# Kernel tuning notes

Hardware: AMD Instinct MI355X
Metric: run time of the kernel (lower is better)

Reference implementation:

```python
import jax, jax.numpy as jnp
from jax import lax
import numpy as np

SEQ, BATCH, IN, H = 512, 256, 180, 8


def _lstm_layer(x, w_ih, w_hh, b_ih, b_hh):
    # x: [S, B, I]; PyTorch gate order: i, f, g, o stacked along 4H
    S, B, _ = x.shape
    Hh = w_hh.shape[1]
    # input contribution for all timesteps at once (one big GEMM)
    xg = jnp.einsum('sbi,gi->sbg', x, w_ih) + b_ih + b_hh  # [S, B, 4H]

    def step(carry, xt):
        h, c = carry
        g = xt + h @ w_hh.T  # [B, 4H]
        i, f, gg, o = jnp.split(g, 4, axis=-1)
        i = jax.nn.sigmoid(i)
        f = jax.nn.sigmoid(f)
        gg = jnp.tanh(gg)
        o = jax.nn.sigmoid(o)
        c = f * c + i * gg
        h = o * jnp.tanh(c)
        return (h, c), h

    init = (jnp.zeros((B, Hh), x.dtype), jnp.zeros((B, Hh), x.dtype))
    _, ys = lax.scan(step, init, xg)
    return ys  # [S, B, H]


def setup_inputs() -> dict:
    key = jax.random.key(0)
    ks = jax.random.split(key, 11)
    s = 1.0 / np.sqrt(H)  # PyTorch LSTM init scale
    return {
        'x': jax.random.normal(ks[0], (SEQ, BATCH, IN), jnp.float32),
        'w_ih0': jax.random.uniform(ks[1], (4 * H, IN), jnp.float32, -s, s),
        'w_hh0': jax.random.uniform(ks[2], (4 * H, H), jnp.float32, -s, s),
        'b_ih0': jax.random.uniform(ks[3], (4 * H,), jnp.float32, -s, s),
        'b_hh0': jax.random.uniform(ks[4], (4 * H,), jnp.float32, -s, s),
        'w_ih1': jax.random.uniform(ks[5], (4 * H, H), jnp.float32, -s, s),
        'w_hh1': jax.random.uniform(ks[6], (4 * H, H), jnp.float32, -s, s),
        'b_ih1': jax.random.uniform(ks[7], (4 * H,), jnp.float32, -s, s),
        'b_hh1': jax.random.uniform(ks[8], (4 * H,), jnp.float32, -s, s),
        'w_reg': jax.random.uniform(ks[9], (2, H), jnp.float32, -s, s),
        'b_reg': jax.random.uniform(ks[10], (2,), jnp.float32, -s, s),
    }


def reference(x, w_ih0, w_hh0, b_ih0, b_hh0, w_ih1, w_hh1, b_ih1, b_hh1, w_reg, b_reg):
    h1 = _lstm_layer(x, w_ih0, w_hh0, b_ih0, b_hh0)   # [S, B, H]
    h2 = _lstm_layer(h1, w_ih1, w_hh1, b_ih1, b_hh1)  # [S, B, H]
    S, B, Hh = h2.shape
    flat = h2.reshape(S * B, Hh)
    return flat @ w_reg.T + b_reg  # [S*B, 2]
```

## Files before the change

kernel.cpp:

```cpp
#include <hip/hip_runtime.h>

#define S_  512
#define B_  256
#define NIN 180

typedef float v2 __attribute__((ext_vector_type(2)));

#define SSIG  -1.4426950408889634f
#define STANH -2.8853900817779268f

#define QP_X1 0xB1
#define QP_X2 0x4E
#define QP_X3 0x1B
#define ROR4  0x124
#define ROR8  0x128

template<int CTRL>
__device__ __forceinline__ float dppf(float x) {
    return __uint_as_float((unsigned)__builtin_amdgcn_update_dpp(
        0, (int)__float_as_uint(x), CTRL, 0xF, 0xF, true));
}

#define ROTS8(h, r) do { \
    r[0] = (h); \
    r[1] = dppf<QP_X1>(h); \
    r[2] = dppf<QP_X2>(h); \
    r[3] = dppf<QP_X3>(h); \
    r[4] = dppf<ROR4>(h); \
    r[5] = dppf<QP_X1>(r[4]); \
    r[6] = dppf<QP_X2>(r[4]); \
    r[7] = dppf<QP_X3>(r[4]); \
} while (0)

__global__ __launch_bounds__(512) void xg_gemm(
    const float* __restrict__ x, const float* __restrict__ w,
    const float* __restrict__ bi, const float* __restrict__ bh,
    float* __restrict__ xg2)
{
    __shared__ float xs[64][181];

    const int tid = threadIdx.x;
    const int s   = blockIdx.x >> 2;
    const int rq  = blockIdx.x & 3;
    const int b0  = rq * 64;

    const float* xsrc = x + ((size_t)s * B_ + b0) * NIN;
    #pragma unroll
    for (int k = 0; k < 6; ++k) {
        int f4 = tid + k * 512;
        if (f4 < 2880) {
            float4 v = *(const float4*)(xsrc + 4 * (size_t)f4);
            int row = f4 / 45;
            int col = (f4 - row * 45) * 4;
            xs[row][col]     = v.x;
            xs[row][col + 1] = v.y;
            xs[row][col + 2] = v.z;
            xs[row][col + 3] = v.w;
        }
    }
    __syncthreads();

    const int wv   = __builtin_amdgcn_readfirstlane(tid >> 6);
    const int qb   = wv & 1;
    const int j0   = (wv >> 1) * 2;
    const int lane = tid & 63;
    const int b    = b0 + lane;

    const int gA0 = qb * 8 + j0;
    const int gB0 = (2 + qb) * 8 + j0;
    const float* wA0 = w + (size_t)gA0 * NIN;
    const float* wA1 = wA0 + NIN;
    const float* wB0 = w + (size_t)gB0 * NIN;
    const float* wB1 = wB0 + NIN;

    float a0 = 0.f, a1 = 0.f, a2 = 0.f, a3 = 0.f;
    #pragma unroll 9
    for (int ii = 0; ii < 45; ++ii) {
        float x0 = xs[lane][4 * ii];
        float x1 = xs[lane][4 * ii + 1];
        float x2 = xs[lane][4 * ii + 2];
        float x3 = xs[lane][4 * ii + 3];
        float4 wa = *(const float4*)(wA0 + 4 * ii);
        float4 wb = *(const float4*)(wB0 + 4 * ii);
        float4 wc = *(const float4*)(wA1 + 4 * ii);
        float4 wd = *(const float4*)(wB1 + 4 * ii);
        a0 = __builtin_fmaf(wa.x, x0, a0); a0 = __builtin_fmaf(wa.y, x1, a0);
        a0 = __builtin_fmaf(wa.z, x2, a0); a0 = __builtin_fmaf(wa.w, x3, a0);
        a1 = __builtin_fmaf(wb.x, x0, a1); a1 = __builtin_fmaf(wb.y, x1, a1);
        a1 = __builtin_fmaf(wb.z, x2, a1); a1 = __builtin_fmaf(wb.w, x3, a1);
        a2 = __builtin_fmaf(wc.x, x0, a2); a2 = __builtin_fmaf(wc.y, x1, a2);
        a2 = __builtin_fmaf(wc.z, x2, a2); a2 = __builtin_fmaf(wc.w, x3, a2);
        a3 = __builtin_fmaf(wd.x, x0, a3); a3 = __builtin_fmaf(wd.y, x1, a3);
        a3 = __builtin_fmaf(wd.z, x2, a3); a3 = __builtin_fmaf(wd.w, x3, a3);
    }

    const float scB = (qb == 0) ? STANH : SSIG;
    float bA0 = bi[gA0] + bh[gA0];
    float bA1 = bi[gA0 + 1] + bh[gA0 + 1];
    float bB0 = bi[gB0] + bh[gB0];
    float bB1 = bi[gB0 + 1] + bh[gB0 + 1];
    float4 o;
    o.x = SSIG * (a0 + bA0);
    o.y = scB  * (a1 + bB0);
    o.z = SSIG * (a2 + bA1);
    o.w = scB  * (a3 + bB1);
    float* dst = xg2 + (((size_t)s * 64 + (b >> 2)) * 64
                        + (b & 3) * 16 + qb * 8 + j0) * 2;
    *(float4*)dst = o;
}

__global__ __launch_bounds__(256, 1) void lstm_scan(
    const float* __restrict__ xg,
    const float* __restrict__ w_hh0,
    const float* __restrict__ w_ih1, const float* __restrict__ w_hh1,
    const float* __restrict__ b_ih1, const float* __restrict__ b_hh1,
    const float* __restrict__ w_reg, const float* __restrict__ b_reg,
    float* __restrict__ out)
{
    __shared__ float ring0[16][64];
    __shared__ float ring1[16][128];
    __shared__ float ring2[16][64];

    const int tid = threadIdx.x;
    const int wid = tid >> 6;
    const int lt  = tid & 63;
    const int j   = lt & 7;
    const int b3  = (lt >> 3) & 1;
    const int cc  = lt >> 4;
    const bool b3z = (b3 == 0);
    const int bid = blockIdx.x;

    const int gA = b3 * 8 + j;
    const int gB = (2 + b3) * 8 + j;
    const float sB_ = b3z ? STANH : SSIG;
    const float aB  = b3z ? 2.0f : 1.0f;
    const float bB  = b3z ? -1.0f : 0.0f;

    auto COMBINE2 = [&](float tA, float tB, float& c, float& h) {
        float m  = tA * tB;
        float mr = dppf<ROR8>(m);
        float fa = dppf<ROR8>(tA);
        float ob = dppf<ROR8>(tB);
        float ig = b3z ? m  : mr;
        float f  = b3z ? fa : tA;
        float o  = b3z ? ob : tB;
        c = __builtin_fmaf(f, c, ig);
        float th = __builtin_fmaf(2.0f, __builtin_amdgcn_rcpf(
            1.0f + __builtin_amdgcn_exp2f(STANH * c)), -1.0f);
        h = o * th;
    };

    if (wid == 0) {
        v2 w0p[8];
        #pragma unroll
        for (int m = 0; m < 8; ++m) {
            int k = j ^ m;
            w0p[m] = v2{SSIG * w_hh0[gA * 8 + k], sB_ * w_hh0[gB * 8 + k]};
        }
        float h0p = 0.f, c0v = 0.f;

        const float* xbase = xg + (size_t)bid * 128 + lt * 2;
        v2 xq[8];
        #pragma unroll
        for (int k = 0; k < 8; ++k) xq[k] = *(const v2*)(xbase + (size_t)k * 8192);

        for (int hh = 0; hh < 64; ++hh) {
            const float* pre = xbase + (size_t)((8 * hh + 8) & 511) * 8192;
            const int sb8 = (hh & 1) * 8;
            #pragma unroll
            for (int k = 0; k < 8; ++k) {
                v2 xc = xq[k];
                xq[k] = *(const v2*)(pre + (size_t)k * 8192);
                float r0[8];
                ROTS8(h0p, r0);
                v2 a0L = __builtin_elementwise_fma(w0p[0], v2{r0[0], r0[0]}, xc);
                v2 a0H = w0p[4] * v2{r0[4], r0[4]};
                #pragma unroll
                for (int m = 1; m < 4; ++m) {
                    a0L = __builtin_elementwise_fma(w0p[m], v2{r0[m], r0[m]}, a0L);
                    a0H = __builtin_elementwise_fma(w0p[m + 4], v2{r0[m + 4], r0[m + 4]}, a0H);
                }
                v2 a0 = a0L + a0H;
                float eA = __builtin_amdgcn_exp2f(a0.x);
                float eB = __builtin_amdgcn_exp2f(a0.y);
                float tA = __builtin_amdgcn_rcpf(1.0f + eA);
                float tB = __builtin_fmaf(aB, __builtin_amdgcn_rcpf(1.0f + eB), bB);
                COMBINE2(tA, tB, c0v, h0p);
                ring0[sb8 + k][lt] = h0p;
                if (k == 3 || k == 7) __syncthreads();
            }
        }
        __syncthreads();
        __syncthreads();
    } else if (wid == 1) {
        v2 wi1p[8];
        #pragma unroll
        for (int m = 0; m < 8; ++m) {
            int k = j ^ m;
            wi1p[m] = v2{SSIG * w_ih1[gA * 8 + k], sB_ * w_ih1[gB * 8 + k]};
        }
        const v2 b1p = v2{SSIG * (b_ih1[gA] + b_hh1[gA]),
                          sB_  * (b_ih1[gB] + b_hh1[gB])};

        __syncthreads();
        for (int p = 1; p <= 128; ++p) {
            const int sb = ((p - 1) & 3) * 4;
            float h0v[4];
            #pragma unroll
            for (int k = 0; k < 4; ++k) h0v[k] = ring0[sb + k][lt];
            #pragma unroll
            for (int k = 0; k < 4; ++k) {
                float r0[8];
                ROTS8(h0v[k], r0);
                v2 a = __builtin_elementwise_fma(wi1p[0], v2{r0[0], r0[0]}, b1p);
                #pragma unroll
                for (int m = 1; m < 8; ++m)
                    a = __builtin_elementwise_fma(wi1p[m], v2{r0[m], r0[m]}, a);
                *(v2*)&ring1[sb + k][lt * 2] = a;
            }
            __syncthreads();
        }
        __syncthreads();
    } else if (wid == 2) {
        v2 wh1p[8];
        #pragma unroll
        for (int m = 0; m < 8; ++m) {
            int k = j ^ m;
            wh1p[m] = v2{SSIG * w_hh1[gA * 8 + k], sB_ * w_hh1[gB * 8 + k]};
        }
        float h1p = 0.f, c1v = 0.f;

        auto BODY4 = [&](int p) {
            const int sb = ((p - 2) & 3) * 4;
            v2 a1in[4];
            #pragma unroll
            for (int k = 0; k < 4; ++k) a1in[k] = *(const v2*)&ring1[sb + k][lt * 2];
            #pragma unroll
            for (int k = 0; k < 4; ++k) {
                float r1[8];
                ROTS8(h1p, r1);
                v2 aL = __builtin_elementwise_fma(wh1p[0], v2{r1[0], r1[0]}, a1in[k]);
                v2 aH = wh1p[4] * v2{r1[4], r1[4]};
                #pragma unroll
                for (int m = 1; m < 4; ++m) {
                    aL = __builtin_elementwise_fma(wh1p[m], v2{r1[m], r1[m]}, aL);
                    aH = __builtin_elementwise_fma(wh1p[m + 4], v2{r1[m + 4], r1[m + 4]}, aH);
                }
                v2 a1 = aL + aH;
                float eA = __builtin_amdgcn_exp2f(a1.x);
                float eB = __builtin_amdgcn_exp2f(a1.y);
                float tA = __builtin_amdgcn_rcpf(1.0f + eA);
                float tB = __builtin_fmaf(aB, __builtin_amdgcn_rcpf(1.0f + eB), bB);
                COMBINE2(tA, tB, c1v, h1p);
                ring2[sb + k][lt] = h1p;
            }
        };

        __syncthreads();
        __syncthreads();
        for (int p = 2; p <= 128; ++p) { BODY4(p); __syncthreads(); }
        BODY4(129);
        __syncthreads();
    } else {
        float wrl[8];
        #pragma unroll
        for (int m = 0; m < 8; ++m) wrl[m] = w_reg[b3 * 8 + (j ^ m)];
        const float br  = b_reg[b3];
        const bool isl  = (j == 0);
        const int  ooff = (bid * 4 + cc) * 2 + b3;

        auto PBODY = [&](int sb, int wbase) {
            float h1v[4];
            #pragma unroll
            for (int k = 0; k < 4; ++k) h1v[k] = ring2[sb + k][lt];
            #pragma unroll
            for (int k = 0; k < 4; ++k) {
                float r1[8];
                ROTS8(h1v[k], r1);
                float pp = br;
                #pragma unroll
                for (int m = 0; m < 8; ++m) pp = __builtin_fmaf(wrl[m], r1[m], pp);
                if (isl) out[(size_t)(wbase + k) * 512 + ooff] = pp;
            }
        };

        __syncthreads();
        __syncthreads();
        __syncthreads();
        for (int p = 3; p <= 129; ++p) {
            PBODY(((p - 3) & 3) * 4, 4 * (p - 3));
            __syncthreads();
        }
        PBODY(12, 508);
    }
}

extern "C" void kernel_launch(void* const* d_in, const int* in_sizes, int n_in,
                              void* d_out, int out_size, void* d_ws, size_t ws_size,
                              hipStream_t stream) {
    (void)in_sizes; (void)n_in; (void)out_size; (void)ws_size;
    const float* x     = (const float*)d_in[0];
    const float* w_ih0 = (const float*)d_in[1];
    const float* w_hh0 = (const float*)d_in[2];
    const float* b_ih0 = (const float*)d_in[3];
    const float* b_hh0 = (const float*)d_in[4];
    const float* w_ih1 = (const float*)d_in[5];
    const float* w_hh1 = (const float*)d_in[6];
    const float* b_ih1 = (const float*)d_in[7];
    const float* b_hh1 = (const float*)d_in[8];
    const float* w_reg = (const float*)d_in[9];
    const float* b_reg = (const float*)d_in[10];
    float* out = (float*)d_out;
    float* xg2 = (float*)d_ws;

    xg_gemm<<<2048, 512, 0, stream>>>(x, w_ih0, b_ih0, b_hh0, xg2);
    lstm_scan<<<64, 256, 0, stream>>>(xg2, w_hh0, w_ih1, w_hh1, b_ih1, b_hh1,
                                      w_reg, b_reg, out);
}
```

Baseline: 114.3 us.

## Fuse input-projection GEMM into scan kernel as producer warps feeding LDS ring

Removes the separate xg_gemm kernel and the global workspace round trip by adding four producer wavefronts to the scan block. These compute the layer-0 input projection for upcoming timesteps and write it into a shared-memory ring consumed by the layer-0 recurrence wave. The fused kernel now uses 512 threads and carries extra barriers to keep the stages aligned. The GEMM now runs on only 64 blocks' worth of producer waves, so it may fall behind the serial recurrence. Barrier counts also have to match exactly across all waves.

```diff
diff --git a/kernel.cpp b/kernel.cpp
--- a/kernel.cpp
+++ b/kernel.cpp
@@ -32,86 +32,10 @@
     r[7] = dppf<QP_X3>(r[4]); \
 } while (0)
 
-__global__ __launch_bounds__(512) void xg_gemm(
-    const float* __restrict__ x, const float* __restrict__ w,
-    const float* __restrict__ bi, const float* __restrict__ bh,
-    float* __restrict__ xg2)
-{
-    __shared__ float xs[64][181];
-
-    const int tid = threadIdx.x;
-    const int s   = blockIdx.x >> 2;
-    const int rq  = blockIdx.x & 3;
-    const int b0  = rq * 64;
-
-    const float* xsrc = x + ((size_t)s * B_ + b0) * NIN;
-    #pragma unroll
-    for (int k = 0; k < 6; ++k) {
-        int f4 = tid + k * 512;
-        if (f4 < 2880) {
-            float4 v = *(const float4*)(xsrc + 4 * (size_t)f4);
-            int row = f4 / 45;
-            int col = (f4 - row * 45) * 4;
-            xs[row][col]     = v.x;
-            xs[row][col + 1] = v.y;
-            xs[row][col + 2] = v.z;
-            xs[row][col + 3] = v.w;
-        }
-    }
-    __syncthreads();
-
-    const int wv   = __builtin_amdgcn_readfirstlane(tid >> 6);
-    const int qb   = wv & 1;
-    const int j0   = (wv >> 1) * 2;
-    const int lane = tid & 63;
-    const int b    = b0 + lane;
-
-    const int gA0 = qb * 8 + j0;
-    const int gB0 = (2 + qb) * 8 + j0;
-    const float* wA0 = w + (size_t)gA0 * NIN;
-    const float* wA1 = wA0 + NIN;
-    const float* wB0 = w + (size_t)gB0 * NIN;
-    const float* wB1 = wB0 + NIN;
-
-    float a0 = 0.f, a1 = 0.f, a2 = 0.f, a3 = 0.f;
-    #pragma unroll 9
-    for (int ii = 0; ii < 45; ++ii) {
-        float x0 = xs[lane][4 * ii];
-        float x1 = xs[lane][4 * ii + 1];
-        float x2 = xs[lane][4 * ii + 2];
-        float x3 = xs[lane][4 * ii + 3];
-        float4 wa = *(const float4*)(wA0 + 4 * ii);
-        float4 wb = *(const float4*)(wB0 + 4 * ii);
-        float4 wc = *(const float4*)(wA1 + 4 * ii);
-        float4 wd = *(const float4*)(wB1 + 4 * ii);
-        a0 = __builtin_fmaf(wa.x, x0, a0); a0 = __builtin_fmaf(wa.y, x1, a0);
-        a0 = __builtin_fmaf(wa.z, x2, a0); a0 = __builtin_fmaf(wa.w, x3, a0);
-        a1 = __builtin_fmaf(wb.x, x0, a1); a1 = __builtin_fmaf(wb.y, x1, a1);
-        a1 = __builtin_fmaf(wb.z, x2, a1); a1 = __builtin_fmaf(wb.w, x3, a1);
-        a2 = __builtin_fmaf(wc.x, x0, a2); a2 = __builtin_fmaf(wc.y, x1, a2);
-        a2 = __builtin_fmaf(wc.z, x2, a2); a2 = __builtin_fmaf(wc.w, x3, a2);
-        a3 = __builtin_fmaf(wd.x, x0, a3); a3 = __builtin_fmaf(wd.y, x1, a3);
-        a3 = __builtin_fmaf(wd.z, x2, a3); a3 = __builtin_fmaf(wd.w, x3, a3);
-    }
-
-    const float scB = (qb == 0) ? STANH : SSIG;
-    float bA0 = bi[gA0] + bh[gA0];
-    float bA1 = bi[gA0 + 1] + bh[gA0 + 1];
-    float bB0 = bi[gB0] + bh[gB0];
-    float bB1 = bi[gB0 + 1] + bh[gB0 + 1];
-    float4 o;
-    o.x = SSIG * (a0 + bA0);
-    o.y = scB  * (a1 + bB0);
-    o.z = SSIG * (a2 + bA1);
-    o.w = scB  * (a3 + bB1);
-    float* dst = xg2 + (((size_t)s * 64 + (b >> 2)) * 64
-                        + (b & 3) * 16 + qb * 8 + j0) * 2;
-    *(float4*)dst = o;
-}
-
-__global__ __launch_bounds__(256, 1) void lstm_scan(
-    const float* __restrict__ xg,
-    const float* __restrict__ w_hh0,
+__global__ __launch_bounds__(512, 1) void lstm_all(
+    const float* __restrict__ x,
+    const float* __restrict__ w_ih0, const float* __restrict__ b_ih0,
+    const float* __restrict__ b_hh0, const float* __restrict__ w_hh0,
     const float* __restrict__ w_ih1, const float* __restrict__ w_hh1,
     const float* __restrict__ b_ih1, const float* __restrict__ b_hh1,
     const float* __restrict__ w_reg, const float* __restrict__ b_reg,
@@ -120,6 +44,9 @@
     __shared__ float ring0[16][64];
     __shared__ float ring1[16][128];
     __shared__ float ring2[16][64];
+    __shared__ float ring3[16][128];
+    __shared__ v2    wpk[16][182];
+    __shared__ float xrow[4][2][4][184];
 
     const int tid = threadIdx.x;
     const int wid = tid >> 6;
@@ -150,6 +77,12 @@
         h = o * th;
     };
 
+    for (int idx = tid; idx < 2880; idx += 512) {
+        int p = idx / 180, i = idx - p * 180;
+        wpk[p][i] = v2{w_ih0[p * 180 + i], w_ih0[(p + 16) * 180 + i]};
+    }
+    __syncthreads();
+
     if (wid == 0) {
         v2 w0p[8];
         #pragma unroll
@@ -158,22 +91,20 @@
             w0p[m] = v2{SSIG * w_hh0[gA * 8 + k], sB_ * w_hh0[gB * 8 + k]};
         }
         float h0p = 0.f, c0v = 0.f;
-
-        const float* xbase = xg + (size_t)bid * 128 + lt * 2;
-        v2 xq[8];
-        #pragma unroll
-        for (int k = 0; k < 8; ++k) xq[k] = *(const v2*)(xbase + (size_t)k * 8192);
-
-        for (int hh = 0; hh < 64; ++hh) {
-            const float* pre = xbase + (size_t)((8 * hh + 8) & 511) * 8192;
-            const int sb8 = (hh & 1) * 8;
-            #pragma unroll
-            for (int k = 0; k < 8; ++k) {
-                v2 xc = xq[k];
-                xq[k] = *(const v2*)(pre + (size_t)k * 8192);
+        __syncthreads();
+        __syncthreads();
+
+        for (int ph = 0; ph < 128; ++ph) {
+            const int sb = (ph & 3) * 4;
+            v2 xq[4];
+            #pragma unroll
+            for (int k = 0; k < 4; ++k)
+                xq[k] = *(const v2*)&ring3[sb + k][lt * 2];
+            #pragma unroll
+            for (int k = 0; k < 4; ++k) {
                 float r0[8];
                 ROTS8(h0p, r0);
-                v2 a0L = __builtin_elementwise_fma(w0p[0], v2{r0[0], r0[0]}, xc);
+                v2 a0L = __builtin_elementwise_fma(w0p[0], v2{r0[0], r0[0]}, xq[k]);
                 v2 a0H = w0p[4] * v2{r0[4], r0[4]};
                 #pragma unroll
                 for (int m = 1; m < 4; ++m) {
@@ -186,9 +117,9 @@
                 float tA = __builtin_amdgcn_rcpf(1.0f + eA);
                 float tB = __builtin_fmaf(aB, __builtin_amdgcn_rcpf(1.0f + eB), bB);
                 COMBINE2(tA, tB, c0v, h0p);
-                ring0[sb8 + k][lt] = h0p;
-                if (k == 3 || k == 7) __syncthreads();
-            }
+                ring0[sb + k][lt] = h0p;
+            }
+            __syncthreads();
         }
         __syncthreads();
         __syncthreads();
@@ -201,6 +132,8 @@
         }
         const v2 b1p = v2{SSIG * (b_ih1[gA] + b_hh1[gA]),
                           sB_  * (b_ih1[gB] + b_hh1[gB])};
+        __syncthreads();
+        __syncthreads();
 
         __syncthreads();
         for (int p = 1; p <= 128; ++p) {
@@ -258,10 +191,12 @@
 
         __syncthreads();
         __syncthreads();
+        __syncthreads();
+        __syncthreads();
         for (int p = 2; p <= 128; ++p) { BODY4(p); __syncthreads(); }
         BODY4(129);
         __syncthreads();
-    } else {
+    } else if (wid == 3) {
         float wrl[8];
         #pragma unroll
         for (int m = 0; m < 8; ++m) wrl[m] = w_reg[b3 * 8 + (j ^ m)];
@@ -287,18 +222,86 @@
         __syncthreads();
         __syncthreads();
         __syncthreads();
+        __syncthreads();
+        __syncthreads();
         for (int p = 3; p <= 129; ++p) {
             PBODY(((p - 3) & 3) * 4, 4 * (p - 3));
             __syncthreads();
         }
         PBODY(12, 508);
+    } else {
+        const int gw = wid - 4;
+        const int bl = lt >> 4;
+        const int p  = lt & 15;
+        const v2 sc = v2{SSIG, (p < 8) ? STANH : SSIG};
+        const v2 bsc = sc * v2{b_ih0[p] + b_hh0[p],
+                               b_ih0[p + 16] + b_hh0[p + 16]};
+
+        auto XLOAD = [&](int r, float4* xr) {
+            const float* src = x + ((size_t)r * B_ + 4 * bid) * NIN;
+            #pragma unroll
+            for (int k = 0; k < 3; ++k) {
+                int f4 = lt + 64 * k;
+                if (f4 < 180) xr[k] = *(const float4*)(src + 4 * f4);
+            }
+        };
+        auto XSTORE = [&](int buf, const float4* xr) {
+            #pragma unroll
+            for (int k = 0; k < 3; ++k) {
+                int f4 = lt + 64 * k;
+                if (f4 < 180) {
+                    int b = f4 / 45, c4 = (f4 - b * 45) * 4;
+                    *(float4*)&xrow[gw][buf][b][c4] = xr[k];
+                }
+            }
+        };
+        auto PROW = [&](int r, int buf) {
+            v2 acc = v2{0.f, 0.f};
+            const float* xr_ = &xrow[gw][buf][bl][0];
+            #pragma unroll 9
+            for (int i4 = 0; i4 < 45; ++i4) {
+                float4 xv = *(const float4*)(xr_ + 4 * i4);
+                v2 w0 = wpk[p][4 * i4];
+                v2 w1 = wpk[p][4 * i4 + 1];
+                v2 w2 = wpk[p][4 * i4 + 2];
+                v2 w3 = wpk[p][4 * i4 + 3];
+                acc = __builtin_elementwise_fma(w0, v2{xv.x, xv.x}, acc);
+                acc = __builtin_elementwise_fma(w1, v2{xv.y, xv.y}, acc);
+                acc = __builtin_elementwise_fma(w2, v2{xv.z, xv.z}, acc);
+                acc = __builtin_elementwise_fma(w3, v2{xv.w, xv.w}, acc);
+            }
+            v2 o = __builtin_elementwise_fma(acc, sc, bsc);
+            *(v2*)&ring3[r & 15][lt * 2] = o;
+        };
+
+        float4 xa[3], xb[3];
+        XLOAD(gw, xa);
+        XLOAD(4 + gw, xb);
+        XSTORE(0, xa);
+        PROW(gw, 0);
+        __syncthreads();
+        XSTORE(1, xb);
+        XLOAD(8 + gw, xa);
+        PROW(4 + gw, 1);
+        __syncthreads();
+        for (int ph = 0; ph <= 125; ++ph) {
+            const int buf = ph & 1;
+            XSTORE(buf, xa);
+            if (ph < 125) XLOAD(4 * ph + 12 + gw, xa);
+            PROW(4 * ph + 8 + gw, buf);
+            __syncthreads();
+        }
+        __syncthreads();
+        __syncthreads();
+        __syncthreads();
+        __syncthreads();
     }
 }
 
 extern "C" void kernel_launch(void* const* d_in, const int* in_sizes, int n_in,
                               void* d_out, int out_size, void* d_ws, size_t ws_size,
                               hipStream_t stream) {
-    (void)in_sizes; (void)n_in; (void)out_size; (void)ws_size;
+    (void)in_sizes; (void)n_in; (void)out_size; (void)d_ws; (void)ws_size;
     const float* x     = (const float*)d_in[0];
     const float* w_ih0 = (const float*)d_in[1];
     const float* w_hh0 = (const float*)d_in[2];
@@ -311,9 +314,8 @@
     const float* w_reg = (const float*)d_in[9];
     const float* b_reg = (const float*)d_in[10];
     float* out = (float*)d_out;
-    float* xg2 = (float*)d_ws;
-
-    xg_gemm<<<2048, 512, 0, stream>>>(x, w_ih0, b_ih0, b_hh0, xg2);
-    lstm_scan<<<64, 256, 0, stream>>>(xg2, w_hh0, w_ih1, w_hh1, b_ih1, b_hh1,
-                                      w_reg, b_reg, out);
+
+    lstm_all<<<64, 512, 0, stream>>>(x, w_ih0, b_ih0, b_hh0, w_hh0,
+                                     w_ih1, w_hh1, b_ih1, b_hh1,
+                                     w_reg, b_reg, out);
 }
```

Result: slower. 423.0 us (+270.0%).
